# Optimization experiments

Hardware: AMD Instinct MI355X
Metric: run time of the kernel (lower is better)

The kernel has to match this reference:

```python
import jax, jax.numpy as jnp
import numpy as np


def _kabsch_rmsd(p, c):
    # p, c: [N, 3]
    pm = jnp.mean(p, axis=0)  # [3]
    cm = jnp.mean(c, axis=0)  # [3]
    # 3x3 cross-covariance
    A = (p - pm).T @ (c - cm)
    U, S, Vt = jnp.linalg.svd(A, full_matrices=False)
    d = jnp.sign(jnp.linalg.det(A))
    # corr_mat = diag([1, 1, d]);  rotation = U @ corr_mat @ Vt
    scale = jnp.concatenate([jnp.ones((2,), dtype=p.dtype), d[None].astype(p.dtype)])
    R = U @ (scale[:, None] * Vt)  # [3,3]
    # translation = pm - R @ cm; aligned coords = (R @ c^T)^T + translation
    aligned = c @ R.T + (pm - R @ cm)
    sq = jnp.sum((p - aligned) ** 2, axis=1)  # [N]
    return jnp.sqrt(jnp.mean(sq))


def setup_inputs() -> dict:
    key = jax.random.key(0)
    k1, k2 = jax.random.split(key)
    B, N = 4096, 2048
    coords_pred = jax.random.normal(k1, (B, N, 3), dtype=jnp.float32)
    coords = jax.random.normal(k2, (B, N, 3), dtype=jnp.float32)
    return {"coords_pred": coords_pred, "coords": coords}


def reference(coords_pred, coords):
    # Batched Kabsch alignment + RMSD; default mode='global', return_all=False
    # -> mean over the per-sample RMSDs.
    rmsds = jax.vmap(_kabsch_rmsd)(coords_pred, coords)  # [B]
    return jnp.mean(rmsds)
```

## Files before the change

kernel.cpp:

```cpp
#include <hip/hip_runtime.h>
#include <math.h>

#define NPTS 2048
#define BLOCK 256
#define WPB 4
#define ITERS 8

__global__ __launch_bounds__(BLOCK, 4) void kabsch_kernel(
    const float* __restrict__ P, const float* __restrict__ C,
    float* __restrict__ rmsd_out, int B) {
  const int wave = threadIdx.x >> 6;
  const int lane = threadIdx.x & 63;
  const int b = blockIdx.x * WPB + wave;
  if (b >= B) return;

  const float4* p4 = (const float4*)(P + (size_t)b * (NPTS * 3));
  const float4* c4 = (const float4*)(C + (size_t)b * (NPTS * 3));

  float acc[17];
#pragma unroll
  for (int i = 0; i < 17; i++) acc[i] = 0.f;

  int base = 3 * lane;
  float4 pa = p4[base], pb = p4[base + 1], pq = p4[base + 2];
  float4 ca = c4[base], cb = c4[base + 1], cq = c4[base + 2];

#pragma unroll
  for (int k = 0; k < ITERS; k++) {
    float4 npa, npb, npq, nca, ncb, ncq;
    if (k < ITERS - 1) {
      const int nb_ = base + 192;
      npa = p4[nb_]; npb = p4[nb_ + 1]; npq = p4[nb_ + 2];
      nca = c4[nb_]; ncb = c4[nb_ + 1]; ncq = c4[nb_ + 2];
    }
    const float Px[4] = {pa.x, pa.w, pb.z, pq.y};
    const float Py[4] = {pa.y, pb.x, pb.w, pq.z};
    const float Pz[4] = {pa.z, pb.y, pq.x, pq.w};
    const float Cx[4] = {ca.x, ca.w, cb.z, cq.y};
    const float Cy[4] = {ca.y, cb.x, cb.w, cq.z};
    const float Cz[4] = {ca.z, cb.y, cq.x, cq.w};
#pragma unroll
    for (int i = 0; i < 4; i++) {
      const float px = Px[i], py = Py[i], pz = Pz[i];
      const float cx = Cx[i], cy = Cy[i], cz = Cz[i];
      acc[0] += px; acc[1] += py; acc[2] += pz;
      acc[3] += cx; acc[4] += cy; acc[5] += cz;
      acc[6] += px * px + py * py + pz * pz;
      acc[7] += cx * cx + cy * cy + cz * cz;
      acc[8]  += px * cx; acc[9]  += px * cy; acc[10] += px * cz;
      acc[11] += py * cx; acc[12] += py * cy; acc[13] += py * cz;
      acc[14] += pz * cx; acc[15] += pz * cy; acc[16] += pz * cz;
    }
    pa = npa; pb = npb; pq = npq;
    ca = nca; cb = ncb; cq = ncq;
    base += 192;
  }

#pragma unroll
  for (int off = 32; off > 0; off >>= 1) {
#pragma unroll
    for (int i = 0; i < 17; i++) acc[i] += __shfl_down(acc[i], off);
  }

  if (lane == 0) {
    double s[17];
#pragma unroll
    for (int i = 0; i < 17; i++) s[i] = (double)acc[i];
    const double invN = 1.0 / (double)NPTS;
    const double spx = s[0], spy = s[1], spz = s[2];
    const double scx = s[3], scy = s[4], scz = s[5];
    const double Ep = s[6] - (spx * spx + spy * spy + spz * spz) * invN;
    const double Ec = s[7] - (scx * scx + scy * scy + scz * scz) * invN;
    const double a00 = s[8]  - spx * scx * invN, a01 = s[9]  - spx * scy * invN, a02 = s[10] - spx * scz * invN;
    const double a10 = s[11] - spy * scx * invN, a11 = s[12] - spy * scy * invN, a12 = s[13] - spy * scz * invN;
    const double a20 = s[14] - spz * scx * invN, a21 = s[15] - spz * scy * invN, a22 = s[16] - spz * scz * invN;
    const double det = a00 * (a11 * a22 - a12 * a21)
                     - a01 * (a10 * a22 - a12 * a20)
                     + a02 * (a10 * a21 - a11 * a20);
    const double b00 = a00 * a00 + a10 * a10 + a20 * a20;
    const double b11 = a01 * a01 + a11 * a11 + a21 * a21;
    const double b22 = a02 * a02 + a12 * a12 + a22 * a22;
    const double b01 = a00 * a01 + a10 * a11 + a20 * a21;
    const double b02 = a00 * a02 + a10 * a12 + a20 * a22;
    const double b12 = a01 * a02 + a11 * a12 + a21 * a22;
    const double q = (b00 + b11 + b22) / 3.0;
    const double p1 = b01 * b01 + b02 * b02 + b12 * b12;
    const double d0 = b00 - q, d1 = b11 - q, d2 = b22 - q;
    const double p2 = d0 * d0 + d1 * d1 + d2 * d2 + 2.0 * p1;
    double e1, e2, e3;
    if (p2 < 1e-30) {
      e1 = e2 = e3 = q;
    } else {
      const double pp = sqrt(p2 / 6.0);
      const double inv = 1.0 / pp;
      const double c00 = d0 * inv, c11 = d1 * inv, c22 = d2 * inv;
      const double c01 = b01 * inv, c02 = b02 * inv, c12 = b12 * inv;
      double r = 0.5 * (c00 * (c11 * c22 - c12 * c12)
                      - c01 * (c01 * c22 - c12 * c02)
                      + c02 * (c01 * c12 - c11 * c02));
      r = fmin(1.0, fmax(-1.0, r));
      const double phi = acos(r) / 3.0;
      e1 = q + 2.0 * pp * cos(phi);
      e3 = q + 2.0 * pp * cos(phi + 2.0943951023931953);
      e2 = 3.0 * q - e1 - e3;
    }
    const double s1 = sqrt(fmax(e1, 0.0));
    const double s2 = sqrt(fmax(e2, 0.0));
    const double s3 = sqrt(fmax(e3, 0.0));
    const double dsign = (det > 0.0) ? 1.0 : ((det < 0.0) ? -1.0 : 0.0);
    const double trRS = s1 + s2 + dsign * s3;
    const double msd = (Ep + Ec - 2.0 * trRS) * invN;
    rmsd_out[b] = (float)sqrt(fmax(msd, 0.0));
  }
}

__global__ __launch_bounds__(BLOCK) void mean_kernel(
    const float* __restrict__ rmsd, float* __restrict__ out, int B) {
  float s = 0.f;
  for (int i = threadIdx.x; i < B; i += BLOCK) s += rmsd[i];
#pragma unroll
  for (int off = 32; off > 0; off >>= 1) s += __shfl_down(s, off);
  __shared__ float sm[BLOCK / 64];
  const int wave = threadIdx.x >> 6, lane = threadIdx.x & 63;
  if (lane == 0) sm[wave] = s;
  __syncthreads();
  if (threadIdx.x == 0) {
    float tot = 0.f;
    for (int w = 0; w < BLOCK / 64; w++) tot += sm[w];
    out[0] = tot / (float)B;
  }
}

extern "C" void kernel_launch(void* const* d_in, const int* in_sizes, int n_in,
                              void* d_out, int out_size, void* d_ws, size_t ws_size,
                              hipStream_t stream) {
  const float* P = (const float*)d_in[0];
  const float* C = (const float*)d_in[1];
  float* out = (float*)d_out;
  float* ws = (float*)d_ws;
  const int B = in_sizes[0] / (NPTS * 3);
  const int grid = (B + WPB - 1) / WPB;
  kabsch_kernel<<<grid, BLOCK, 0, stream>>>(P, C, ws, B);
  mean_kernel<<<1, BLOCK, 0, stream>>>(ws, out, B);
}
```

Baseline: 223.2 us.

## Stage each sample via direct global-to-LDS loads with one block per sample

Reassigns work from one wave per sample to one 256-thread block per sample. Both point clouds are loaded straight into shared memory with global_load_lds, then reduced with per-thread strided reads and a cross-wave shared-memory reduction. The per-sample eigen/SVD epilogue also moves from double to float. This aims to raise memory-level parallelism and drop slow FP64 work, at the cost of 48KB of LDS per block, an extra barrier, and lower epilogue precision.

```diff
diff --git a/kernel.cpp b/kernel.cpp
--- a/kernel.cpp
+++ b/kernel.cpp
@@ -2,58 +2,54 @@
 #include <math.h>
 
 #define NPTS 2048
+#define NF4 (NPTS * 3 / 4)
 #define BLOCK 256
-#define WPB 4
-#define ITERS 8
+#define CHUNKS (NF4 / BLOCK)
+#define PPT (NPTS / BLOCK)
 
-__global__ __launch_bounds__(BLOCK, 4) void kabsch_kernel(
+__global__ __launch_bounds__(BLOCK, 3) void kabsch_kernel(
     const float* __restrict__ P, const float* __restrict__ C,
     float* __restrict__ rmsd_out, int B) {
-  const int wave = threadIdx.x >> 6;
-  const int lane = threadIdx.x & 63;
-  const int b = blockIdx.x * WPB + wave;
-  if (b >= B) return;
+  __shared__ float4 sP[NF4];
+  __shared__ float4 sC[NF4];
+  __shared__ float red[BLOCK / 64][17];
 
+  const int b = blockIdx.x;
+  const int t = threadIdx.x;
   const float4* p4 = (const float4*)(P + (size_t)b * (NPTS * 3));
   const float4* c4 = (const float4*)(C + (size_t)b * (NPTS * 3));
+
+#pragma unroll
+  for (int c = 0; c < CHUNKS; c++) {
+    const int idx = c * BLOCK + t;
+    __builtin_amdgcn_global_load_lds(
+        (const __attribute__((address_space(1))) void*)(p4 + idx),
+        (__attribute__((address_space(3))) void*)(&sP[idx]), 16, 0, 0);
+    __builtin_amdgcn_global_load_lds(
+        (const __attribute__((address_space(1))) void*)(c4 + idx),
+        (__attribute__((address_space(3))) void*)(&sC[idx]), 16, 0, 0);
+  }
+  __syncthreads();
+
+  const float* Pf = (const float*)sP;
+  const float* Cf = (const float*)sC;
 
   float acc[17];
 #pragma unroll
   for (int i = 0; i < 17; i++) acc[i] = 0.f;
 
-  int base = 3 * lane;
-  float4 pa = p4[base], pb = p4[base + 1], pq = p4[base + 2];
-  float4 ca = c4[base], cb = c4[base + 1], cq = c4[base + 2];
-
 #pragma unroll
-  for (int k = 0; k < ITERS; k++) {
-    float4 npa, npb, npq, nca, ncb, ncq;
-    if (k < ITERS - 1) {
-      const int nb_ = base + 192;
-      npa = p4[nb_]; npb = p4[nb_ + 1]; npq = p4[nb_ + 2];
-      nca = c4[nb_]; ncb = c4[nb_ + 1]; ncq = c4[nb_ + 2];
-    }
-    const float Px[4] = {pa.x, pa.w, pb.z, pq.y};
-    const float Py[4] = {pa.y, pb.x, pb.w, pq.z};
-    const float Pz[4] = {pa.z, pb.y, pq.x, pq.w};
-    const float Cx[4] = {ca.x, ca.w, cb.z, cq.y};
-    const float Cy[4] = {ca.y, cb.x, cb.w, cq.z};
-    const float Cz[4] = {ca.z, cb.y, cq.x, cq.w};
-#pragma unroll
-    for (int i = 0; i < 4; i++) {
-      const float px = Px[i], py = Py[i], pz = Pz[i];
-      const float cx = Cx[i], cy = Cy[i], cz = Cz[i];
-      acc[0] += px; acc[1] += py; acc[2] += pz;
-      acc[3] += cx; acc[4] += cy; acc[5] += cz;
-      acc[6] += px * px + py * py + pz * pz;
-      acc[7] += cx * cx + cy * cy + cz * cz;
-      acc[8]  += px * cx; acc[9]  += px * cy; acc[10] += px * cz;
-      acc[11] += py * cx; acc[12] += py * cy; acc[13] += py * cz;
-      acc[14] += pz * cx; acc[15] += pz * cy; acc[16] += pz * cz;
-    }
-    pa = npa; pb = npb; pq = npq;
-    ca = nca; cb = ncb; cq = ncq;
-    base += 192;
+  for (int k = 0; k < PPT; k++) {
+    const int pt = k * BLOCK + t;
+    const float px = Pf[3 * pt], py = Pf[3 * pt + 1], pz = Pf[3 * pt + 2];
+    const float cx = Cf[3 * pt], cy = Cf[3 * pt + 1], cz = Cf[3 * pt + 2];
+    acc[0] += px; acc[1] += py; acc[2] += pz;
+    acc[3] += cx; acc[4] += cy; acc[5] += cz;
+    acc[6] += px * px + py * py + pz * pz;
+    acc[7] += cx * cx + cy * cy + cz * cz;
+    acc[8]  += px * cx; acc[9]  += px * cy; acc[10] += px * cz;
+    acc[11] += py * cx; acc[12] += py * cy; acc[13] += py * cz;
+    acc[14] += pz * cx; acc[15] += pz * cy; acc[16] += pz * cz;
   }
 
 #pragma unroll
@@ -61,56 +57,63 @@
 #pragma unroll
     for (int i = 0; i < 17; i++) acc[i] += __shfl_down(acc[i], off);
   }
+  const int wave = t >> 6, lane = t & 63;
+  if (lane == 0) {
+#pragma unroll
+    for (int i = 0; i < 17; i++) red[wave][i] = acc[i];
+  }
+  __syncthreads();
 
-  if (lane == 0) {
-    double s[17];
+  if (t == 0) {
+    float s[17];
 #pragma unroll
-    for (int i = 0; i < 17; i++) s[i] = (double)acc[i];
-    const double invN = 1.0 / (double)NPTS;
-    const double spx = s[0], spy = s[1], spz = s[2];
-    const double scx = s[3], scy = s[4], scz = s[5];
-    const double Ep = s[6] - (spx * spx + spy * spy + spz * spz) * invN;
-    const double Ec = s[7] - (scx * scx + scy * scy + scz * scz) * invN;
-    const double a00 = s[8]  - spx * scx * invN, a01 = s[9]  - spx * scy * invN, a02 = s[10] - spx * scz * invN;
-    const double a10 = s[11] - spy * scx * invN, a11 = s[12] - spy * scy * invN, a12 = s[13] - spy * scz * invN;
-    const double a20 = s[14] - spz * scx * invN, a21 = s[15] - spz * scy * invN, a22 = s[16] - spz * scz * invN;
-    const double det = a00 * (a11 * a22 - a12 * a21)
-                     - a01 * (a10 * a22 - a12 * a20)
-                     + a02 * (a10 * a21 - a11 * a20);
-    const double b00 = a00 * a00 + a10 * a10 + a20 * a20;
-    const double b11 = a01 * a01 + a11 * a11 + a21 * a21;
-    const double b22 = a02 * a02 + a12 * a12 + a22 * a22;
-    const double b01 = a00 * a01 + a10 * a11 + a20 * a21;
-    const double b02 = a00 * a02 + a10 * a12 + a20 * a22;
-    const double b12 = a01 * a02 + a11 * a12 + a21 * a22;
-    const double q = (b00 + b11 + b22) / 3.0;
-    const double p1 = b01 * b01 + b02 * b02 + b12 * b12;
-    const double d0 = b00 - q, d1 = b11 - q, d2 = b22 - q;
-    const double p2 = d0 * d0 + d1 * d1 + d2 * d2 + 2.0 * p1;
-    double e1, e2, e3;
-    if (p2 < 1e-30) {
+    for (int i = 0; i < 17; i++)
+      s[i] = red[0][i] + red[1][i] + red[2][i] + red[3][i];
+    const float invN = 1.0f / (float)NPTS;
+    const float spx = s[0], spy = s[1], spz = s[2];
+    const float scx = s[3], scy = s[4], scz = s[5];
+    const float Ep = s[6] - (spx * spx + spy * spy + spz * spz) * invN;
+    const float Ec = s[7] - (scx * scx + scy * scy + scz * scz) * invN;
+    const float a00 = s[8]  - spx * scx * invN, a01 = s[9]  - spx * scy * invN, a02 = s[10] - spx * scz * invN;
+    const float a10 = s[11] - spy * scx * invN, a11 = s[12] - spy * scy * invN, a12 = s[13] - spy * scz * invN;
+    const float a20 = s[14] - spz * scx * invN, a21 = s[15] - spz * scy * invN, a22 = s[16] - spz * scz * invN;
+    const float det = a00 * (a11 * a22 - a12 * a21)
+                    - a01 * (a10 * a22 - a12 * a20)
+                    + a02 * (a10 * a21 - a11 * a20);
+    const float b00 = a00 * a00 + a10 * a10 + a20 * a20;
+    const float b11 = a01 * a01 + a11 * a11 + a21 * a21;
+    const float b22 = a02 * a02 + a12 * a12 + a22 * a22;
+    const float b01 = a00 * a01 + a10 * a11 + a20 * a21;
+    const float b02 = a00 * a02 + a10 * a12 + a20 * a22;
+    const float b12 = a01 * a02 + a11 * a12 + a21 * a22;
+    const float q = (b00 + b11 + b22) * (1.f / 3.f);
+    const float p1 = b01 * b01 + b02 * b02 + b12 * b12;
+    const float d0 = b00 - q, d1 = b11 - q, d2 = b22 - q;
+    const float p2 = d0 * d0 + d1 * d1 + d2 * d2 + 2.f * p1;
+    float e1, e2, e3;
+    if (p2 < 1e-20f) {
       e1 = e2 = e3 = q;
     } else {
-      const double pp = sqrt(p2 / 6.0);
-      const double inv = 1.0 / pp;
-      const double c00 = d0 * inv, c11 = d1 * inv, c22 = d2 * inv;
-      const double c01 = b01 * inv, c02 = b02 * inv, c12 = b12 * inv;
-      double r = 0.5 * (c00 * (c11 * c22 - c12 * c12)
+      const float pp = sqrtf(p2 * (1.f / 6.f));
+      const float inv = 1.f / pp;
+      const float c00 = d0 * inv, c11 = d1 * inv, c22 = d2 * inv;
+      const float c01 = b01 * inv, c02 = b02 * inv, c12 = b12 * inv;
+      float r = 0.5f * (c00 * (c11 * c22 - c12 * c12)
                       - c01 * (c01 * c22 - c12 * c02)
                       + c02 * (c01 * c12 - c11 * c02));
-      r = fmin(1.0, fmax(-1.0, r));
-      const double phi = acos(r) / 3.0;
-      e1 = q + 2.0 * pp * cos(phi);
-      e3 = q + 2.0 * pp * cos(phi + 2.0943951023931953);
-      e2 = 3.0 * q - e1 - e3;
+      r = fminf(1.f, fmaxf(-1.f, r));
+      const float phi = acosf(r) * (1.f / 3.f);
+      e1 = q + 2.f * pp * cosf(phi);
+      e3 = q + 2.f * pp * cosf(phi + 2.0943951023931953f);
+      e2 = 3.f * q - e1 - e3;
     }
-    const double s1 = sqrt(fmax(e1, 0.0));
-    const double s2 = sqrt(fmax(e2, 0.0));
-    const double s3 = sqrt(fmax(e3, 0.0));
-    const double dsign = (det > 0.0) ? 1.0 : ((det < 0.0) ? -1.0 : 0.0);
-    const double trRS = s1 + s2 + dsign * s3;
-    const double msd = (Ep + Ec - 2.0 * trRS) * invN;
-    rmsd_out[b] = (float)sqrt(fmax(msd, 0.0));
+    const float s1 = sqrtf(fmaxf(e1, 0.f));
+    const float s2 = sqrtf(fmaxf(e2, 0.f));
+    const float s3 = sqrtf(fmaxf(e3, 0.f));
+    const float dsign = (det > 0.f) ? 1.f : ((det < 0.f) ? -1.f : 0.f);
+    const float trRS = s1 + s2 + dsign * s3;
+    const float msd = (Ep + Ec - 2.f * trRS) * invN;
+    rmsd_out[b] = sqrtf(fmaxf(msd, 0.f));
   }
 }
 
@@ -139,7 +142,6 @@
   float* out = (float*)d_out;
   float* ws = (float*)d_ws;
   const int B = in_sizes[0] / (NPTS * 3);
-  const int grid = (B + WPB - 1) / WPB;
-  kabsch_kernel<<<grid, BLOCK, 0, stream>>>(P, C, ws, B);
+  kabsch_kernel<<<B, BLOCK, 0, stream>>>(P, C, ws, B);
   mean_kernel<<<1, BLOCK, 0, stream>>>(ws, out, B);
 }
```

New measurement: 219.2 us. About the same (-1.8%).
